# Kernel tuning notes

Measured on AMD Instinct MI355X. Metric: run time of the kernel, lower is better.

The kernel has to match this reference:

```python
import jax, jax.numpy as jnp
import numpy as np

B, P, G = 64, 512, 64      # batch of independent nets, populations, generator inputs
N = P + G                   # presynaptic channels per population
H = 32                      # neuron-MLP hidden width
DT = 0.1                    # integration step (ms)
EREV_MIN, EREV_MAX = -75.0, 0.0


def setup_inputs() -> dict:
    key = jax.random.key(0)
    ks = jax.random.split(key, 16)
    state = jax.random.uniform(ks[0], (B, P), dtype=jnp.float32)          # prev firing rates
    inp = jax.random.uniform(ks[1], (B, G), dtype=jnp.float32)            # generator rates
    R = jnp.ones((B, P, N), dtype=jnp.float32)                            # recovered resources
    U = jnp.zeros((B, P, N), dtype=jnp.float32)                           # utilization
    A = jnp.zeros((B, P, N), dtype=jnp.float32)                           # active resources
    gsyn_max = 2.0 * jax.random.uniform(ks[2], (P, N), dtype=jnp.float32)
    pconn = jax.random.uniform(ks[3], (P, N), dtype=jnp.float32)
    Uinc = 0.1 + 0.5 * jax.random.uniform(ks[4], (P, N), dtype=jnp.float32)
    tau_r = 100.0 + 400.0 * jax.random.uniform(ks[5], (P, N), dtype=jnp.float32)  # recovery (ms)
    tau_f = 10.0 + 50.0 * jax.random.uniform(ks[6], (P, N), dtype=jnp.float32)    # facilitation
    tau_d = 2.0 + 5.0 * jax.random.uniform(ks[7], (P, N), dtype=jnp.float32)      # decay
    Erev = jnp.where(jax.random.uniform(ks[8], (P, N)) > 0.5, 0.0, -75.0).astype(jnp.float32)
    mask = jnp.ones((P, N), dtype=bool)                                   # is_connected_mask
    Cm = 0.5 + 2.0 * jax.random.uniform(ks[9], (P,), dtype=jnp.float32)
    W1 = 0.5 * jax.random.normal(ks[10], (P, 2, H), dtype=jnp.float32)
    b1 = 0.5 * jax.random.normal(ks[11], (P, H), dtype=jnp.float32)
    W2 = 0.5 * jax.random.normal(ks[12], (P, H, 1), dtype=jnp.float32)
    b2 = 0.5 * jax.random.normal(ks[13], (P, 1), dtype=jnp.float32)
    return {"state": state, "inp": inp, "R": R, "U": U, "A": A,
            "gsyn_max": gsyn_max, "pconn": pconn, "Uinc": Uinc,
            "tau_r": tau_r, "tau_f": tau_f, "tau_d": tau_d,
            "Erev": Erev, "mask": mask, "Cm": Cm,
            "W1": W1, "b1": b1, "W2": W2, "b2": b2}


def reference(state, inp, R, U, A, gsyn_max, pconn, Uinc, tau_r, tau_f, tau_d,
              Erev, mask, Cm, W1, b1, W2, b2):
    # --- TimeStepLayer.call: concat prev state with generator input -> full presyn vector
    x = jnp.concatenate([state, inp], axis=-1)                  # [B, N]
    SR = x[:, None, :] * pconn                                  # [B, P, N] spike prob per conn

    # --- TsodycsMarkramSynapse one Euler step (all populations fused)
    e_d = jnp.exp(-DT / tau_d)
    e_r = jnp.exp(-DT / tau_r)
    e_f = jnp.exp(-DT / tau_f)
    tau1r = jnp.where(tau_d != tau_r, tau_d / (tau_d - tau_r), 1e-13)
    a_dec = A * e_d
    r_dec = 1.0 + (R - 1.0 + tau1r * U) * e_r - tau1r * U
    u_dec = U * e_f
    u0 = u_dec + Uinc * (1.0 - u_dec) * SR                      # new utilization
    a0 = a_dec + u0 * r_dec * SR                                # new active fraction

    # --- synaptic drive features per population
    g = gsyn_max * a0 * mask                                    # [B, P, N]
    g_tot = jnp.sum(g, axis=-1)                                 # [B, P]
    E_eff = jnp.sum(g * Erev, axis=-1) / (g_tot + 1e-8)
    E_norm = (E_eff - EREV_MIN) / (EREV_MAX - EREV_MIN)
    g_norm = g_tot / (g_tot + Cm[None, :])
    feat = jnp.stack([E_norm, g_norm], axis=-1)                 # [B, P, 2]

    # --- frozen per-population neuron net (square activation, sigmoid rate)
    h = jnp.square(jnp.einsum('bpf,pfh->bph', feat, W1) + b1)   # [B, P, H]
    out = jax.nn.sigmoid(jnp.einsum('bph,pho->bpo', h, W2) + b2)[..., 0]  # [B, P]
    return out
```

## Files before the change

kernel.cpp:

```cpp
#include <hip/hip_runtime.h>

#define PP 512
#define GG 64
#define NN 576
#define HH 32

#define DERIVE(i, PC, UI, TR, TF, TD, GS, ER)                                \
  {                                                                          \
    float e_r  = __expf(-0.1f * __builtin_amdgcn_rcpf(TR));                  \
    float e_f  = __expf(-0.1f * __builtin_amdgcn_rcpf(TF));                  \
    float e_d  = __expf(-0.1f * __builtin_amdgcn_rcpf(TD));                  \
    float diff = (TD) - (TR);                                                \
    float t1r  = (diff != 0.0f) ? (TD) * __builtin_amdgcn_rcpf(diff)         \
                                : 1e-13f;                                    \
    pc[i] = (PC);                                                            \
    up[i] = (UI) * (PC);                                                     \
    ef[i] = e_f;                                                             \
    er[i] = e_r;                                                             \
    c1[i] = t1r * (e_r - 1.0f);                                              \
    ed[i] = e_d;                                                             \
    gs[i] = (GS);                                                            \
    gEv[i] = (GS) * (ER);                                                    \
  }

#define STEP(i, Rv, Uv, Av, Xv)                                              \
  {                                                                          \
    float sr   = (Xv) * pc[i];                                               \
    float udec = (Uv) * ef[i];                                               \
    float upx  = up[i] * (Xv);                                               \
    float u0   = udec + upx * (1.0f - udec);                                 \
    float rdec = 1.0f + ((Rv) - 1.0f) * er[i] + c1[i] * (Uv);                \
    float a0   = (Av) * ed[i] + u0 * rdec * sr;                              \
    gt = fmaf(gs[i], a0, gt);                                                \
    ge = fmaf(gEv[i], a0, ge);                                               \
  }

__global__ __launch_bounds__(256, 3)
void timestep_kernel(const float* __restrict__ state,
                     const float* __restrict__ inp,
                     const float* __restrict__ R,
                     const float* __restrict__ U,
                     const float* __restrict__ A,
                     const float* __restrict__ gsyn_max,
                     const float* __restrict__ pconn,
                     const float* __restrict__ Uinc,
                     const float* __restrict__ tau_r,
                     const float* __restrict__ tau_f,
                     const float* __restrict__ tau_d,
                     const float* __restrict__ Erev,
                     const float* __restrict__ Cm,
                     const float* __restrict__ W1,
                     const float* __restrict__ b1,
                     const float* __restrict__ W2,
                     const float* __restrict__ b2,
                     float* __restrict__ out)
{
    const int tid  = threadIdx.x;
    const int lane = tid & 63;
    const int wave = tid >> 6;
    const int p    = blockIdx.x >> 1;
    const int half = blockIdx.x & 1;

    float pc[9], up[9], ef[9], er[9], c1[9], ed[9], gs[9], gEv[9];

    const int prow = p * NN;
    #pragma unroll
    for (int c = 0; c < 2; ++c) {
        const int f4 = (prow >> 2) + c * 64 + lane;
        float4 v_pc = ((const float4*)pconn)[f4];
        float4 v_ui = ((const float4*)Uinc)[f4];
        float4 v_tr = ((const float4*)tau_r)[f4];
        float4 v_tf = ((const float4*)tau_f)[f4];
        float4 v_td = ((const float4*)tau_d)[f4];
        float4 v_gs = ((const float4*)gsyn_max)[f4];
        float4 v_er = ((const float4*)Erev)[f4];
        DERIVE(c * 4 + 0, v_pc.x, v_ui.x, v_tr.x, v_tf.x, v_td.x, v_gs.x, v_er.x)
        DERIVE(c * 4 + 1, v_pc.y, v_ui.y, v_tr.y, v_tf.y, v_td.y, v_gs.y, v_er.y)
        DERIVE(c * 4 + 2, v_pc.z, v_ui.z, v_tr.z, v_tf.z, v_td.z, v_gs.z, v_er.z)
        DERIVE(c * 4 + 3, v_pc.w, v_ui.w, v_tr.w, v_tf.w, v_td.w, v_gs.w, v_er.w)
    }
    {
        const int o = prow + 512 + lane;
        DERIVE(8, pconn[o], Uinc[o], tau_r[o], tau_f[o], tau_d[o],
               gsyn_max[o], Erev[o])
    }

    const int   j   = lane & 31;
    const float w1a = W1[p * 64 + j];
    const float w1b = W1[p * 64 + 32 + j];
    const float b1j = b1[p * 32 + j];
    const float w2j = W2[p * 32 + j];
    const float b2p = b2[p];
    const float cmp = Cm[p];

    const int bend = half * 32 + 32;
    for (int b = half * 32 + wave; b < bend; b += 4) {
        const size_t rbase = ((size_t)b * PP + p) * (size_t)NN;
        const size_t r4    = rbase >> 2;
        const int    s4    = (b * PP) >> 2;
        float gt = 0.0f, ge = 0.0f;

        #pragma unroll
        for (int c = 0; c < 2; ++c) {
            const size_t o4 = r4 + (size_t)(c * 64 + lane);
            float4 Rv = ((const float4*)R)[o4];
            float4 Uv = ((const float4*)U)[o4];
            float4 Av = ((const float4*)A)[o4];
            float4 Xv = ((const float4*)state)[s4 + c * 64 + lane];
            STEP(c * 4 + 0, Rv.x, Uv.x, Av.x, Xv.x)
            STEP(c * 4 + 1, Rv.y, Uv.y, Av.y, Xv.y)
            STEP(c * 4 + 2, Rv.z, Uv.z, Av.z, Xv.z)
            STEP(c * 4 + 3, Rv.w, Uv.w, Av.w, Xv.w)
        }
        {
            const size_t o = rbase + 512 + (size_t)lane;
            float Rs = R[o];
            float Us = U[o];
            float As = A[o];
            float Xs = inp[b * GG + lane];
            STEP(8, Rs, Us, As, Xs)
        }

        #pragma unroll
        for (int m = 32; m >= 1; m >>= 1) {
            gt += __shfl_xor(gt, m, 64);
            ge += __shfl_xor(ge, m, 64);
        }

        float Eeff = ge / (gt + 1e-8f);
        float En   = (Eeff + 75.0f) / 75.0f;
        float gn   = gt / (gt + cmp);
        float pre  = fmaf(En, w1a, fmaf(gn, w1b, b1j));
        float hv   = pre * pre;
        float v    = hv * w2j;
        #pragma unroll
        for (int m = 16; m >= 1; m >>= 1) v += __shfl_xor(v, m, 64);
        float s = v + b2p;
        float r = 1.0f / (1.0f + __expf(-s));
        if (lane == 0) out[(size_t)b * PP + p] = r;
    }
}

extern "C" void kernel_launch(void* const* d_in, const int* in_sizes, int n_in,
                              void* d_out, int out_size, void* d_ws, size_t ws_size,
                              hipStream_t stream) {
    const float* state = (const float*)d_in[0];
    const float* inp   = (const float*)d_in[1];
    const float* R     = (const float*)d_in[2];
    const float* U     = (const float*)d_in[3];
    const float* A     = (const float*)d_in[4];
    const float* gsyn  = (const float*)d_in[5];
    const float* pconn = (const float*)d_in[6];
    const float* Uinc  = (const float*)d_in[7];
    const float* taur  = (const float*)d_in[8];
    const float* tauf  = (const float*)d_in[9];
    const float* taud  = (const float*)d_in[10];
    const float* Erev  = (const float*)d_in[11];
    const float* Cm    = (const float*)d_in[13];
    const float* W1    = (const float*)d_in[14];
    const float* b1    = (const float*)d_in[15];
    const float* W2    = (const float*)d_in[16];
    const float* b2    = (const float*)d_in[17];
    float* out = (float*)d_out;

    hipLaunchKernelGGL(timestep_kernel, dim3(1024), dim3(256), 0, stream,
                       state, inp, R, U, A, gsyn, pconn, Uinc, taur, tauf, taud,
                       Erev, Cm, W1, b1, W2, b2, out);
}
```

Before: 253.1 us.

## Split batches over four blocks per population and process two batches per wave

Each population is now split across four blocks of 16 batch rows instead of two blocks of 32, which doubles the grid, and launch bounds are raised to four blocks per CU. Each wave handles two batch rows at a time, interleaving their loads and reductions to raise memory-level parallelism. The per-population constant derivation (exp/rcp of tau parameters) is now repeated in twice as many blocks. Exact divisions in the epilogue are replaced with hardware reciprocals, which slightly changes precision.

```diff
diff --git a/kernel.cpp b/kernel.cpp
--- a/kernel.cpp
+++ b/kernel.cpp
@@ -3,7 +3,6 @@
 #define PP 512
 #define GG 64
 #define NN 576
-#define HH 32
 
 #define DERIVE(i, PC, UI, TR, TF, TD, GS, ER)                                \
   {                                                                          \
@@ -23,7 +22,7 @@
     gEv[i] = (GS) * (ER);                                                    \
   }
 
-#define STEP(i, Rv, Uv, Av, Xv)                                              \
+#define STEP(i, Rv, Uv, Av, Xv, GT, GE)                                      \
   {                                                                          \
     float sr   = (Xv) * pc[i];                                               \
     float udec = (Uv) * ef[i];                                               \
@@ -31,11 +30,11 @@
     float u0   = udec + upx * (1.0f - udec);                                 \
     float rdec = 1.0f + ((Rv) - 1.0f) * er[i] + c1[i] * (Uv);                \
     float a0   = (Av) * ed[i] + u0 * rdec * sr;                              \
-    gt = fmaf(gs[i], a0, gt);                                                \
-    ge = fmaf(gEv[i], a0, ge);                                               \
+    GT = fmaf(gs[i], a0, GT);                                                \
+    GE = fmaf(gEv[i], a0, GE);                                               \
   }
 
-__global__ __launch_bounds__(256, 3)
+__global__ __launch_bounds__(256, 4)
 void timestep_kernel(const float* __restrict__ state,
                      const float* __restrict__ inp,
                      const float* __restrict__ R,
@@ -58,8 +57,8 @@
     const int tid  = threadIdx.x;
     const int lane = tid & 63;
     const int wave = tid >> 6;
-    const int p    = blockIdx.x >> 1;
-    const int half = blockIdx.x & 1;
+    const int p    = blockIdx.x >> 2;
+    const int bg   = blockIdx.x & 3;
 
     float pc[9], up[9], ef[9], er[9], c1[9], ed[9], gs[9], gEv[9];
 
@@ -93,51 +92,75 @@
     const float b2p = b2[p];
     const float cmp = Cm[p];
 
-    const int bend = half * 32 + 32;
-    for (int b = half * 32 + wave; b < bend; b += 4) {
-        const size_t rbase = ((size_t)b * PP + p) * (size_t)NN;
-        const size_t r4    = rbase >> 2;
-        const int    s4    = (b * PP) >> 2;
-        float gt = 0.0f, ge = 0.0f;
+    const int bbase = bg * 16 + wave * 4;
+    #pragma unroll
+    for (int pass = 0; pass < 2; ++pass) {
+        const int b0 = bbase + pass * 2;
+        const int b1i = b0 + 1;
+        const size_t r0 = ((size_t)b0 * PP + p) * (size_t)NN;
+        const size_t r1 = ((size_t)b1i * PP + p) * (size_t)NN;
+        float gt0 = 0.0f, ge0 = 0.0f, gt1 = 0.0f, ge1 = 0.0f;
 
         #pragma unroll
         for (int c = 0; c < 2; ++c) {
-            const size_t o4 = r4 + (size_t)(c * 64 + lane);
-            float4 Rv = ((const float4*)R)[o4];
-            float4 Uv = ((const float4*)U)[o4];
-            float4 Av = ((const float4*)A)[o4];
-            float4 Xv = ((const float4*)state)[s4 + c * 64 + lane];
-            STEP(c * 4 + 0, Rv.x, Uv.x, Av.x, Xv.x)
-            STEP(c * 4 + 1, Rv.y, Uv.y, Av.y, Xv.y)
-            STEP(c * 4 + 2, Rv.z, Uv.z, Av.z, Xv.z)
-            STEP(c * 4 + 3, Rv.w, Uv.w, Av.w, Xv.w)
+            const int off = c * 64 + lane;
+            float4 Ra = ((const float4*)R)[(r0 >> 2) + off];
+            float4 Rb = ((const float4*)R)[(r1 >> 2) + off];
+            float4 Ua = ((const float4*)U)[(r0 >> 2) + off];
+            float4 Ub = ((const float4*)U)[(r1 >> 2) + off];
+            float4 Aa = ((const float4*)A)[(r0 >> 2) + off];
+            float4 Ab = ((const float4*)A)[(r1 >> 2) + off];
+            float4 Xa = ((const float4*)state)[((b0 * PP) >> 2) + off];
+            float4 Xb = ((const float4*)state)[((b1i * PP) >> 2) + off];
+            STEP(c * 4 + 0, Ra.x, Ua.x, Aa.x, Xa.x, gt0, ge0)
+            STEP(c * 4 + 1, Ra.y, Ua.y, Aa.y, Xa.y, gt0, ge0)
+            STEP(c * 4 + 2, Ra.z, Ua.z, Aa.z, Xa.z, gt0, ge0)
+            STEP(c * 4 + 3, Ra.w, Ua.w, Aa.w, Xa.w, gt0, ge0)
+            STEP(c * 4 + 0, Rb.x, Ub.x, Ab.x, Xb.x, gt1, ge1)
+            STEP(c * 4 + 1, Rb.y, Ub.y, Ab.y, Xb.y, gt1, ge1)
+            STEP(c * 4 + 2, Rb.z, Ub.z, Ab.z, Xb.z, gt1, ge1)
+            STEP(c * 4 + 3, Rb.w, Ub.w, Ab.w, Xb.w, gt1, ge1)
         }
         {
-            const size_t o = rbase + 512 + (size_t)lane;
-            float Rs = R[o];
-            float Us = U[o];
-            float As = A[o];
-            float Xs = inp[b * GG + lane];
-            STEP(8, Rs, Us, As, Xs)
+            const size_t oa = r0 + 512 + (size_t)lane;
+            const size_t ob = r1 + 512 + (size_t)lane;
+            float Rs0 = R[oa], Us0 = U[oa], As0 = A[oa];
+            float Rs1 = R[ob], Us1 = U[ob], As1 = A[ob];
+            float Xs0 = inp[b0 * GG + lane];
+            float Xs1 = inp[b1i * GG + lane];
+            STEP(8, Rs0, Us0, As0, Xs0, gt0, ge0)
+            STEP(8, Rs1, Us1, As1, Xs1, gt1, ge1)
         }
 
         #pragma unroll
         for (int m = 32; m >= 1; m >>= 1) {
-            gt += __shfl_xor(gt, m, 64);
-            ge += __shfl_xor(ge, m, 64);
+            gt0 += __shfl_xor(gt0, m, 64);
+            gt1 += __shfl_xor(gt1, m, 64);
+            ge0 += __shfl_xor(ge0, m, 64);
+            ge1 += __shfl_xor(ge1, m, 64);
         }
 
-        float Eeff = ge / (gt + 1e-8f);
-        float En   = (Eeff + 75.0f) / 75.0f;
-        float gn   = gt / (gt + cmp);
-        float pre  = fmaf(En, w1a, fmaf(gn, w1b, b1j));
-        float hv   = pre * pre;
-        float v    = hv * w2j;
+        float En0 = (ge0 * __builtin_amdgcn_rcpf(gt0 + 1e-8f) + 75.0f) * (1.0f / 75.0f);
+        float En1 = (ge1 * __builtin_amdgcn_rcpf(gt1 + 1e-8f) + 75.0f) * (1.0f / 75.0f);
+        float gn0 = gt0 * __builtin_amdgcn_rcpf(gt0 + cmp);
+        float gn1 = gt1 * __builtin_amdgcn_rcpf(gt1 + cmp);
+        float pre0 = fmaf(En0, w1a, fmaf(gn0, w1b, b1j));
+        float pre1 = fmaf(En1, w1a, fmaf(gn1, w1b, b1j));
+        float v0 = pre0 * pre0 * w2j;
+        float v1 = pre1 * pre1 * w2j;
         #pragma unroll
-        for (int m = 16; m >= 1; m >>= 1) v += __shfl_xor(v, m, 64);
-        float s = v + b2p;
-        float r = 1.0f / (1.0f + __expf(-s));
-        if (lane == 0) out[(size_t)b * PP + p] = r;
+        for (int m = 16; m >= 1; m >>= 1) {
+            v0 += __shfl_xor(v0, m, 64);
+            v1 += __shfl_xor(v1, m, 64);
+        }
+        float s0 = v0 + b2p;
+        float s1 = v1 + b2p;
+        float o0 = __builtin_amdgcn_rcpf(1.0f + __expf(-s0));
+        float o1 = __builtin_amdgcn_rcpf(1.0f + __expf(-s1));
+        if (lane == 0) {
+            out[(size_t)b0 * PP + p]  = o0;
+            out[(size_t)b1i * PP + p] = o1;
+        }
     }
 }
 
@@ -163,7 +186,7 @@
     const float* b2    = (const float*)d_in[17];
     float* out = (float*)d_out;
 
-    hipLaunchKernelGGL(timestep_kernel, dim3(1024), dim3(256), 0, stream,
+    hipLaunchKernelGGL(timestep_kernel, dim3(2048), dim3(256), 0, stream,
                        state, inp, R, U, A, gsyn, pconn, Uinc, taur, tauf, taud,
                        Erev, Cm, W1, b1, W2, b2, out);
 }
```

Result: no change. 258.2 us (+2.0%).
